# Kernel tuning notes

Measured on AMD Instinct MI355X. Metric: run time of the kernel, lower is better.

## Reference

```python
import jax, jax.numpy as jnp
import numpy as np

N, E, R = 50000, 320000, 3
IN, HID, OUT = 768, 256, 64
NEG_SLOPE = 0.2


def _rgat_conv(x, src, dst, edge_type, W, q, k, bias):
    # x: [N, HID]; W: [R, HID, HID]; q,k: [HID, 1]; bias: [HID]
    n = x.shape[0]
    xw = jnp.einsum('nc,rco->rno', x, W)          # [R, N, HID] per-relation transform
    out_i = xw[edge_type, dst]                      # [E, HID] transformed target feats
    out_j = xw[edge_type, src]                      # [E, HID] transformed source feats
    alpha = jax.nn.leaky_relu(out_i @ q + out_j @ k, NEG_SLOPE)  # [E, 1]
    # across-relation segment softmax over destination nodes (PyG softmax semantics)
    m = jax.ops.segment_max(alpha, dst, num_segments=n)          # [N, 1]
    ea = jnp.exp(alpha - m[dst])
    denom = jax.ops.segment_sum(ea, dst, num_segments=n)         # [N, 1]
    a = ea / (denom[dst] + 1e-16)                                # [E, 1]
    out = jax.ops.segment_sum(a * out_j, dst, num_segments=n)    # [N, HID]
    return out + bias


def setup_inputs() -> dict:
    key = jax.random.key(0)
    ks = jax.random.split(key, 16)
    g = lambda k, shape, fan: (jax.random.normal(k, shape, jnp.float32) / np.float32(np.sqrt(fan)))
    return {
        'x': jax.random.normal(ks[0], (N, IN), jnp.float32),
        'edge_index': jax.random.randint(ks[1], (2, E), 0, N),
        'edge_type': jax.random.randint(ks[2], (E,), 0, R),
        'w_in': g(ks[3], (IN, HID), IN), 'b_in': jnp.zeros((HID,), jnp.float32),
        'conv1_w': g(ks[4], (R, HID, HID), HID),
        'conv1_q': g(ks[5], (HID, 1), HID),
        'conv1_k': g(ks[6], (HID, 1), HID),
        'conv1_b': jnp.zeros((HID,), jnp.float32),
        'conv2_w': g(ks[7], (R, HID, HID), HID),
        'conv2_q': g(ks[8], (HID, 1), HID),
        'conv2_k': g(ks[9], (HID, 1), HID),
        'conv2_b': jnp.zeros((HID,), jnp.float32),
        'w_out': g(ks[10], (HID, OUT), HID), 'b_out': jnp.zeros((OUT,), jnp.float32),
        'w_cls': g(ks[11], (OUT, 2), OUT), 'b_cls': jnp.zeros((2,), jnp.float32),
    }


def reference(x, edge_index, edge_type, w_in, b_in,
              conv1_w, conv1_q, conv1_k, conv1_b,
              conv2_w, conv2_q, conv2_k, conv2_b,
              w_out, b_out, w_cls, b_cls):
    src, dst = edge_index[0], edge_index[1]
    h = jax.nn.relu(x @ w_in + b_in)                                  # [N, HID]
    h = _rgat_conv(h, src, dst, edge_type, conv1_w, conv1_q, conv1_k, conv1_b)
    h = _rgat_conv(h, src, dst, edge_type, conv2_w, conv2_q, conv2_k, conv2_b)
    h = jax.nn.relu(h @ w_out + b_out)                                # [N, OUT]
    return h @ w_cls + b_cls                                          # [N, 2]
```

## Files before the change

### kernel.cpp

```cpp
#include <hip/hip_runtime.h>
#include <hip/hip_bf16.h>

#define RG86_NN 50000
#define RG86_NE 320000
#define RG86_NR 3
#define RG86_DIN 768
#define RG86_HID 256
#define RG86_OUT 64

typedef __bf16 rg_bv8 __attribute__((ext_vector_type(8)));
typedef short rg_sv8 __attribute__((ext_vector_type(8)));
typedef float rg_fv4 __attribute__((ext_vector_type(4)));
typedef unsigned int rg_u32;

static __device__ float rg_b2f(unsigned short u) {
  return __uint_as_float(((unsigned int)u) << 16);
}
static __device__ unsigned short rg_f2b(float f) {
  unsigned int u = __float_as_uint(f);
  u += 0x7FFFu + ((u >> 16) & 1u);
  return (unsigned short)(u >> 16);
}

static __device__ __forceinline__ void rg_gl16(const void* g, void* lds_wave_base) {
  __builtin_amdgcn_global_load_lds(
      (const __attribute__((address_space(1))) rg_u32*)(unsigned long long)(uintptr_t)g,
      (__attribute__((address_space(3))) rg_u32*)(unsigned int)(uintptr_t)lds_wave_base,
      16, 0, 0);
}

__global__ void RGATModel_86371792322702_kernel() {}

__global__ void rg_castT(const float* in, unsigned short* out, int rows, int cols) {
  int i = blockIdx.x * 256 + threadIdx.x;
  if (i < rows * cols) {
    int r = i / cols, c = i % cols;
    out[(size_t)c * rows + r] = rg_f2b(in[i]);
  }
}

__global__ void rg_castT3(const float* in, unsigned short* out) {
  int i = blockIdx.x * 256 + threadIdx.x;
  if (i < RG86_NR * RG86_HID * RG86_HID) {
    int r = i >> 16, j = i & 65535;
    int row = j >> 8, col = j & 255;
    out[(r << 16) + (col << 8) + row] = rg_f2b(in[i]);
  }
}

__global__ void rg_wqk(const float* W, const float* q, const float* k,
                       float* wq, float* wk) {
  int lane = threadIdx.x & 63;
  int p = blockIdx.x * 4 + (threadIdx.x >> 6);
  if (p >= RG86_NR * RG86_HID) return;
  const float* wr = W + (size_t)p * RG86_HID;
  float qv = 0.f, kv = 0.f;
  for (int j = lane; j < RG86_HID; j += 64) {
    float w = wr[j];
    qv += w * q[j];
    kv += w * k[j];
  }
  for (int o = 32; o >= 1; o >>= 1) { qv += __shfl_xor(qv, o); kv += __shfl_xor(kv, o); }
  if (lane == 0) { wq[p] = qv; wk[p] = kv; }
}

__global__ void rg_qk2(const unsigned short* h, const float* wq, const float* wk,
                       float* qd, float* kd) {
  int lane = threadIdx.x & 63;
  int n = blockIdx.x * 4 + (threadIdx.x >> 6);
  if (n >= RG86_NN) return;
  ushort4 hv = *(const ushort4*)(h + (size_t)n * RG86_HID + lane * 4);
  float h0 = rg_b2f(hv.x), h1 = rg_b2f(hv.y), h2 = rg_b2f(hv.z), h3 = rg_b2f(hv.w);
  float acc[6];
#pragma unroll
  for (int r = 0; r < RG86_NR; r++) {
    const float* wqr = wq + r * RG86_HID + lane * 4;
    const float* wkr = wk + r * RG86_HID + lane * 4;
    acc[r] = h0 * wqr[0] + h1 * wqr[1] + h2 * wqr[2] + h3 * wqr[3];
    acc[3 + r] = h0 * wkr[0] + h1 * wkr[1] + h2 * wkr[2] + h3 * wkr[3];
  }
#pragma unroll
  for (int j = 0; j < 6; j++)
    for (int o = 32; o >= 1; o >>= 1) acc[j] += __shfl_xor(acc[j], o);
  if (lane == 0) {
#pragma unroll
    for (int r = 0; r < RG86_NR; r++) {
      qd[r * RG86_NN + n] = acc[r];
      kd[r * RG86_NN + n] = acc[3 + r];
    }
  }
}

__global__ __launch_bounds__(256) void rg_gemm2(
    const unsigned short* A, const unsigned short* Bt, const float* bias,
    unsigned short* C, int M, int N, int K, int relu, int split) {
  __shared__ unsigned short sA[128 * 64];
  __shared__ unsigned short sB[64 * 64];
  int tid = threadIdx.x;
  int wv = tid >> 6, lane = tid & 63;
  int nwg = gridDim.x;
  int q = nwg >> 3, rres = nwg & 7;
  int xcd = blockIdx.x & 7, jj = blockIdx.x >> 3;
  int wg = (xcd < rres ? xcd * (q + 1) : rres * (q + 1) + (xcd - rres) * q) + jj;
  int ntiles = N >> 6;
  int mt = wg / ntiles, nt = wg - mt * ntiles;
  int m0 = mt * 128, n0 = nt * 64;
  int frow = lane & 15, fhi = lane >> 4;
  rg_fv4 acc[2][4] = {};
  for (int k0 = 0; k0 < K; k0 += 64) {
#pragma unroll
    for (int i = 0; i < 4; i++) {
      int idx = i * 256 + tid;
      int r = idx >> 3, s = idx & 7;
      int gr = m0 + r;
      if (gr >= M) gr = M - 1;
      const unsigned short* gp = A + (size_t)gr * K + k0 + ((s ^ (r & 7)) << 3);
      rg_gl16(gp, (char*)sA + (size_t)(i * 256 + wv * 64) * 16);
    }
#pragma unroll
    for (int i = 0; i < 2; i++) {
      int idx = i * 256 + tid;
      int r = idx >> 3, s = idx & 7;
      const unsigned short* gp = Bt + (size_t)(n0 + r) * K + k0 + ((s ^ (r & 7)) << 3);
      rg_gl16(gp, (char*)sB + (size_t)(i * 256 + wv * 64) * 16);
    }
    __syncthreads();
#pragma unroll
    for (int ks = 0; ks < 2; ks++) {
      rg_bv8 af[2], bf[4];
#pragma unroll
      for (int mf = 0; mf < 2; mf++) {
        int r = wv * 32 + mf * 16 + frow;
        int slot = (ks * 4 + fhi) ^ (r & 7);
        af[mf] = *(const rg_bv8*)((const char*)sA + r * 128 + slot * 16);
      }
#pragma unroll
      for (int nf = 0; nf < 4; nf++) {
        int r = nf * 16 + frow;
        int slot = (ks * 4 + fhi) ^ (r & 7);
        bf[nf] = *(const rg_bv8*)((const char*)sB + r * 128 + slot * 16);
      }
#pragma unroll
      for (int mf = 0; mf < 2; mf++)
#pragma unroll
        for (int nf = 0; nf < 4; nf++)
          acc[mf][nf] = __builtin_amdgcn_mfma_f32_16x16x32_bf16(af[mf], bf[nf],
                                                                acc[mf][nf], 0, 0, 0);
    }
    __syncthreads();
  }
#pragma unroll
  for (int mf = 0; mf < 2; mf++) {
#pragma unroll
    for (int nf = 0; nf < 4; nf++) {
      int col = n0 + nf * 16 + frow;
      float bv = bias ? bias[col] : 0.f;
#pragma unroll
      for (int r = 0; r < 4; r++) {
        int row = m0 + wv * 32 + mf * 16 + fhi * 4 + r;
        if (row < M) {
          float v = acc[mf][nf][r] + bv;
          if (relu && v < 0.f) v = 0.f;
          if (split)
            C[((size_t)(col >> 8) * RG86_NN + row) * 256 + (col & 255)] = rg_f2b(v);
          else
            C[(size_t)row * N + col] = rg_f2b(v);
        }
      }
    }
  }
}

__global__ __launch_bounds__(256) void rg_gemm2w(
    const unsigned short* A, const unsigned short* Bt,
    unsigned short* C, int M, int N, int K) {
  __shared__ unsigned short sA[128 * 64];
  __shared__ unsigned short sB[128 * 64];
  int tid = threadIdx.x;
  int wv = tid >> 6, lane = tid & 63;
  int nwg = gridDim.x;
  int q = nwg >> 3, rres = nwg & 7;
  int xcd = blockIdx.x & 7, jj = blockIdx.x >> 3;
  int wg = (xcd < rres ? xcd * (q + 1) : rres * (q + 1) + (xcd - rres) * q) + jj;
  int ntiles = N >> 7;
  int mt = wg / ntiles, nt = wg - mt * ntiles;
  int m0 = mt * 128, n0 = nt * 128;
  int frow = lane & 15, fhi = lane >> 4;
  rg_fv4 acc[2][8] = {};
  for (int k0 = 0; k0 < K; k0 += 64) {
#pragma unroll
    for (int i = 0; i < 4; i++) {
      int idx = i * 256 + tid;
      int r = idx >> 3, s = idx & 7;
      int gr = m0 + r;
      if (gr >= M) gr = M - 1;
      const unsigned short* gp = A + (size_t)gr * K + k0 + ((s ^ (r & 7)) << 3);
      rg_gl16(gp, (char*)sA + (size_t)(i * 256 + wv * 64) * 16);
    }
#pragma unroll
    for (int i = 0; i < 4; i++) {
      int idx = i * 256 + tid;
      int r = idx >> 3, s = idx & 7;
      const unsigned short* gp = Bt + (size_t)(n0 + r) * K + k0 + ((s ^ (r & 7)) << 3);
      rg_gl16(gp, (char*)sB + (size_t)(i * 256 + wv * 64) * 16);
    }
    __syncthreads();
#pragma unroll
    for (int ks = 0; ks < 2; ks++) {
      rg_bv8 af[2], bf[8];
#pragma unroll
      for (int mf = 0; mf < 2; mf++) {
        int r = wv * 32 + mf * 16 + frow;
        int slot = (ks * 4 + fhi) ^ (r & 7);
        af[mf] = *(const rg_bv8*)((const char*)sA + r * 128 + slot * 16);
      }
#pragma unroll
      for (int nf = 0; nf < 8; nf++) {
        int r = nf * 16 + frow;
        int slot = (ks * 4 + fhi) ^ (r & 7);
        bf[nf] = *(const rg_bv8*)((const char*)sB + r * 128 + slot * 16);
      }
#pragma unroll
      for (int mf = 0; mf < 2; mf++)
#pragma unroll
        for (int nf = 0; nf < 8; nf++)
          acc[mf][nf] = __builtin_amdgcn_mfma_f32_16x16x32_bf16(af[mf], bf[nf],
                                                                acc[mf][nf], 0, 0, 0);
    }
    __syncthreads();
  }
#pragma unroll
  for (int mf = 0; mf < 2; mf++) {
#pragma unroll
    for (int nf = 0; nf < 8; nf++) {
      int col = n0 + nf * 16 + frow;
#pragma unroll
      for (int r = 0; r < 4; r++) {
        int row = m0 + wv * 32 + mf * 16 + fhi * 4 + r;
        if (row < M)
          C[((size_t)(col >> 8) * RG86_NN + row) * 256 + (col & 255)] =
              rg_f2b(acc[mf][nf][r]);
      }
    }
  }
}

__global__ __launch_bounds__(256) void rg_gemm2f(
    const float* A, const unsigned short* Bt, const float* bias,
    unsigned short* C, int M, int N, int K, int relu) {
  __shared__ float sA[128 * 64];
  __shared__ unsigned short sB[64 * 64];
  int tid = threadIdx.x;
  int wv = tid >> 6, lane = tid & 63;
  int nwg = gridDim.x;
  int q = nwg >> 3, rres = nwg & 7;
  int xcd = blockIdx.x & 7, jj = blockIdx.x >> 3;
  int wg = (xcd < rres ? xcd * (q + 1) : rres * (q + 1) + (xcd - rres) * q) + jj;
  int ntiles = N >> 6;
  int mt = wg / ntiles, nt = wg - mt * ntiles;
  int m0 = mt * 128, n0 = nt * 64;
  int frow = lane & 15, fhi = lane >> 4;
  rg_fv4 acc[2][4] = {};
  for (int k0 = 0; k0 < K; k0 += 64) {
#pragma unroll
    for (int i = 0; i < 2; i++) {
      int idx = i * 256 + tid;
      int r = idx >> 3, s = idx & 7;
      const unsigned short* gp = Bt + (size_t)(n0 + r) * K + k0 + ((s ^ (r & 7)) << 3);
      rg_gl16(gp, (char*)sB + (size_t)(i * 256 + wv * 64) * 16);
    }
#pragma unroll
    for (int i = 0; i < 8; i++) {
      int idx = i * 256 + tid;
      int r = idx >> 4, hs = idx & 15;
      int gr = m0 + r;
      if (gr >= M) gr = M - 1;
      const float* gp = A + (size_t)gr * K + k0 +
                        ((((hs >> 1) ^ (r & 7)) << 3) + ((hs & 1) << 2));
      rg_gl16(gp, (char*)sA + (size_t)(i * 256 + wv * 64) * 16);
    }
    __syncthreads();
#pragma unroll
    for (int ks = 0; ks < 2; ks++) {
      rg_bv8 af[2], bf[4];
#pragma unroll
      for (int mf = 0; mf < 2; mf++) {
        int r = wv * 32 + mf * 16 + frow;
        int sp = (ks * 4 + fhi) ^ (r & 7);
        const float* ap = sA + r * 64 + sp * 8;
        float4 f0 = *(const float4*)ap;
        float4 f1 = *(const float4*)(ap + 4);
        rg_sv8 av;
        av[0] = (short)rg_f2b(f0.x); av[1] = (short)rg_f2b(f0.y);
        av[2] = (short)rg_f2b(f0.z); av[3] = (short)rg_f2b(f0.w);
        av[4] = (short)rg_f2b(f1.x); av[5] = (short)rg_f2b(f1.y);
        av[6] = (short)rg_f2b(f1.z); av[7] = (short)rg_f2b(f1.w);
        af[mf] = *(rg_bv8*)&av;
      }
#pragma unroll
      for (int nf = 0; nf < 4; nf++) {
        int r = nf * 16 + frow;
        int slot = (ks * 4 + fhi) ^ (r & 7);
        bf[nf] = *(const rg_bv8*)((const char*)sB + r * 128 + slot * 16);
      }
#pragma unroll
      for (int mf = 0; mf < 2; mf++)
#pragma unroll
        for (int nf = 0; nf < 4; nf++)
          acc[mf][nf] = __builtin_amdgcn_mfma_f32_16x16x32_bf16(af[mf], bf[nf],
                                                                acc[mf][nf], 0, 0, 0);
    }
    __syncthreads();
  }
#pragma unroll
  for (int mf = 0; mf < 2; mf++) {
#pragma unroll
    for (int nf = 0; nf < 4; nf++) {
      int col = n0 + nf * 16 + frow;
      float bv = bias ? bias[col] : 0.f;
#pragma unroll
      for (int r = 0; r < 4; r++) {
        int row = m0 + wv * 32 + mf * 16 + fhi * 4 + r;
        if (row < M) {
          float v = acc[mf][nf][r] + bv;
          if (relu && v < 0.f) v = 0.f;
          C[(size_t)row * N + col] = rg_f2b(v);
        }
      }
    }
  }
}

__global__ void rg_hist(const int* d, int* counts) {
  int e = blockIdx.x * 256 + threadIdx.x;
  if (e < RG86_NE) atomicAdd(&counts[d[e]], 1);
}

__global__ void rg_scan1(const int* counts, int* tmp, int* bsum, int n) {
  int b = blockIdx.x, t = threadIdx.x;
  int base = b * 1024 + t * 4;
  int v0 = 0, v1 = 0, v2 = 0, v3 = 0;
  if (base + 3 < n) {
    int4 v = *(const int4*)(counts + base);
    v0 = v.x; v1 = v.y; v2 = v.z; v3 = v.w;
  } else {
    if (base + 0 < n) v0 = counts[base + 0];
    if (base + 1 < n) v1 = counts[base + 1];
    if (base + 2 < n) v2 = counts[base + 2];
    if (base + 3 < n) v3 = counts[base + 3];
  }
  int tsum = v0 + v1 + v2 + v3;
  int lane = t & 63, wave = t >> 6;
  int s = tsum;
  for (int off = 1; off < 64; off <<= 1) {
    int u = __shfl_up(s, off);
    if (lane >= off) s += u;
  }
  __shared__ int wsum[4];
  if (lane == 63) wsum[wave] = s;
  __syncthreads();
  int woff = 0;
  for (int w = 0; w < wave; w++) woff += wsum[w];
  int excl = woff + s - tsum;
  int e0 = excl, e1 = e0 + v0, e2 = e1 + v1, e3 = e2 + v2;
  if (base + 3 < n) {
    *(int4*)(tmp + base) = make_int4(e0, e1, e2, e3);
  } else {
    if (base + 0 < n) tmp[base + 0] = e0;
    if (base + 1 < n) tmp[base + 1] = e1;
    if (base + 2 < n) tmp[base + 2] = e2;
    if (base + 3 < n) tmp[base + 3] = e3;
  }
  if (t == 255) bsum[b] = woff + s;
}

__global__ void rg_scan2(int* bsum, int* rowptr, int nb, int n) {
  int lane = threadIdx.x;
  int v = (lane < nb) ? bsum[lane] : 0;
  int s = v;
  for (int off = 1; off < 64; off <<= 1) {
    int u = __shfl_up(s, off);
    if (lane >= off) s += u;
  }
  if (lane < nb) bsum[lane] = s - v;
  if (lane == 63) rowptr[n] = s;
}

__global__ void rg_scan3(const int* bsum, int* rowptr, int* cursor, int n) {
  int b = blockIdx.x, t = threadIdx.x;
  int base = b * 1024 + t * 4;
  int off = bsum[b];
  if (base + 3 < n) {
    int4 v = *(const int4*)(cursor + base);
    int4 o = make_int4(v.x + off, v.y + off, v.z + off, v.w + off);
    *(int4*)(rowptr + base) = o;
    *(int4*)(cursor + base) = o;
  } else {
    for (int j = 0; j < 4; j++)
      if (base + j < n) {
        int o = cursor[base + j] + off;
        rowptr[base + j] = o;
        cursor[base + j] = o;
      }
  }
}

__global__ void rg_scatter(const int* d, int* cursor, int* perm) {
  int e = blockIdx.x * 256 + threadIdx.x;
  if (e < RG86_NE) perm[atomicAdd(&cursor[d[e]], 1)] = e;
}

__global__ void rg_edge(const int* perm, const int* src, const int* dst,
                        const int* et, const float* qd, const float* kd,
                        float* alphap, int* srcrel) {
  int i = blockIdx.x * 256 + threadIdx.x;
  if (i >= RG86_NE) return;
  int e = perm[i];
  int t = et[e], sv = src[e], dv = dst[e];
  float al = qd[t * RG86_NN + dv] + kd[t * RG86_NN + sv];
  al = al > 0.f ? al : 0.2f * al;
  alphap[i] = al;
  srcrel[i] = t * RG86_NN + sv;
}

__global__ void rg_agg(const int* rowptr, const float* alphap, const int* srcrel,
                       const unsigned short* xw, const float* bias,
                       unsigned short* out) {
  __shared__ float sw[4][64];
  __shared__ int ssrc[4][64];
  int lane = threadIdx.x & 63;
  int wv = threadIdx.x >> 6;
  int node = blockIdx.x * 4 + wv;
  if (node >= RG86_NN) return;
  int s0 = rowptr[node], s1 = rowptr[node + 1];
  int c0 = lane * 4;
  float a0 = 0.f, a1 = 0.f, a2 = 0.f, a3 = 0.f;
  if (s1 > s0) {
    float m = -1e30f;
    for (int bs = s0; bs < s1; bs += 64) {
      int i = bs + lane;
      float al = (i < s1) ? alphap[i] : -1e30f;
      m = fmaxf(m, al);
    }
    for (int o = 32; o >= 1; o >>= 1) m = fmaxf(m, __shfl_xor(m, o));
    float den = 0.f;
    for (int bs = s0; bs < s1; bs += 64) {
      int i = bs + lane;
      if (i < s1) den += __expf(alphap[i] - m);
    }
    for (int o = 32; o >= 1; o >>= 1) den += __shfl_xor(den, o);
    float inv = 1.f / (den + 1e-16f);
    for (int bs = s0; bs < s1; bs += 64) {
      int i = bs + lane;
      int nch = s1 - bs; if (nch > 64) nch = 64;
      float w = 0.f; int sr = 0;
      if (i < s1) { w = __expf(alphap[i] - m) * inv; sr = srcrel[i]; }
      sw[wv][lane] = w;
      ssrc[wv][lane] = sr;
#pragma unroll 4
      for (int j = 0; j < nch; j++) {
        float wj = sw[wv][j];
        ushort4 v = *(const ushort4*)(xw + (size_t)ssrc[wv][j] * RG86_HID + c0);
        a0 += wj * rg_b2f(v.x);
        a1 += wj * rg_b2f(v.y);
        a2 += wj * rg_b2f(v.z);
        a3 += wj * rg_b2f(v.w);
      }
    }
  }
  unsigned short* op = out + (size_t)node * RG86_HID + c0;
  op[0] = rg_f2b(a0 + bias[c0 + 0]);
  op[1] = rg_f2b(a1 + bias[c0 + 1]);
  op[2] = rg_f2b(a2 + bias[c0 + 2]);
  op[3] = rg_f2b(a3 + bias[c0 + 3]);
}

__global__ void rg_cls(const unsigned short* h4, const float* wc, const float* bc,
                       float* out) {
  int n = blockIdx.x * 256 + threadIdx.x;
  if (n >= RG86_NN) return;
  float a0 = bc[0], a1 = bc[1];
  const unsigned short* hr = h4 + (size_t)n * RG86_OUT;
  for (int j = 0; j < RG86_OUT; j++) {
    float h = rg_b2f(hr[j]);
    a0 += h * wc[j * 2 + 0];
    a1 += h * wc[j * 2 + 1];
  }
  out[n * 2 + 0] = a0;
  out[n * 2 + 1] = a1;
}

extern "C" void kernel_launch(void* const* d_in, const int* in_sizes, int n_in,
                              void* d_out, int out_size, void* d_ws, size_t ws_size,
                              hipStream_t stream) {
  (void)in_sizes; (void)n_in; (void)out_size;
  const float* x = (const float*)d_in[0];
  const int* ei = (const int*)d_in[1];
  const int* etp = (const int*)d_in[2];
  const float* w_in = (const float*)d_in[3];
  const float* b_in = (const float*)d_in[4];
  const float* c1w = (const float*)d_in[5];
  const float* c1q = (const float*)d_in[6];
  const float* c1k = (const float*)d_in[7];
  const float* c1b = (const float*)d_in[8];
  const float* c2w = (const float*)d_in[9];
  const float* c2q = (const float*)d_in[10];
  const float* c2k = (const float*)d_in[11];
  const float* c2b = (const float*)d_in[12];
  const float* w_out = (const float*)d_in[13];
  const float* b_out = (const float*)d_in[14];
  const float* w_cls = (const float*)d_in[15];
  const float* b_cls = (const float*)d_in[16];
  const int* esrc = ei;
  const int* edst = ei + RG86_NE;

  char* base = (char*)d_ws;
  size_t off = 0;
  unsigned short* xw = (unsigned short*)(base + off);
  off += (size_t)RG86_NR * RG86_NN * RG86_HID * 2;
  unsigned short* h1b = (unsigned short*)(base + off); off += (size_t)RG86_NN * RG86_HID * 2;
  unsigned short* h2b = (unsigned short*)(base + off); off += (size_t)RG86_NN * RG86_HID * 2;
  unsigned short* h4b = (unsigned short*)(base + off); off += (size_t)RG86_NN * RG86_OUT * 2;
  unsigned short* w_inT = (unsigned short*)(base + off); off += (size_t)RG86_DIN * RG86_HID * 2;
  unsigned short* c1wT = (unsigned short*)(base + off); off += (size_t)RG86_NR * RG86_HID * RG86_HID * 2;
  unsigned short* c2wT = (unsigned short*)(base + off); off += (size_t)RG86_NR * RG86_HID * RG86_HID * 2;
  unsigned short* w_outT = (unsigned short*)(base + off); off += (size_t)RG86_HID * RG86_OUT * 2;
  float* qd = (float*)(base + off); off += (size_t)RG86_NR * RG86_NN * 4;
  float* kd = (float*)(base + off); off += (size_t)RG86_NR * RG86_NN * 4;
  float* wq1 = (float*)(base + off); off += (size_t)RG86_NR * RG86_HID * 4;
  float* wk1 = (float*)(base + off); off += (size_t)RG86_NR * RG86_HID * 4;
  float* wq2 = (float*)(base + off); off += (size_t)RG86_NR * RG86_HID * 4;
  float* wk2 = (float*)(base + off); off += (size_t)RG86_NR * RG86_HID * 4;
  int* counts = (int*)(base + off); off += (size_t)RG86_NN * 4;
  int* rowptr = (int*)(base + off); off += (size_t)(RG86_NN + 4) * 4;
  int* cursor = (int*)(base + off); off += (size_t)RG86_NN * 4;
  int* perm = (int*)(base + off); off += (size_t)RG86_NE * 4;
  int* bsum = (int*)(base + off); off += (size_t)64 * 4;
  float* alphap = (float*)(base + off); off += (size_t)RG86_NE * 4;
  int* srcrel = (int*)(base + off); off += (size_t)RG86_NE * 4;
  if (off > ws_size) return;

  int mt128 = (RG86_NN + 127) / 128;
  int nsb = (RG86_NN + 1023) / 1024;

  rg_castT<<<(RG86_DIN * RG86_HID + 255) / 256, 256, 0, stream>>>(
      w_in, w_inT, RG86_DIN, RG86_HID);
  rg_castT3<<<(RG86_NR * RG86_HID * RG86_HID + 255) / 256, 256, 0, stream>>>(c1w, c1wT);
  rg_castT3<<<(RG86_NR * RG86_HID * RG86_HID + 255) / 256, 256, 0, stream>>>(c2w, c2wT);
  rg_castT<<<(RG86_HID * RG86_OUT + 255) / 256, 256, 0, stream>>>(
      w_out, w_outT, RG86_HID, RG86_OUT);
  rg_wqk<<<(RG86_NR * RG86_HID + 3) / 4, 256, 0, stream>>>(c1w, c1q, c1k, wq1, wk1);
  rg_wqk<<<(RG86_NR * RG86_HID + 3) / 4, 256, 0, stream>>>(c2w, c2q, c2k, wq2, wk2);

  rg_gemm2f<<<mt128 * 4, 256, 0, stream>>>(x, w_inT, b_in, h1b,
                                           RG86_NN, RG86_HID, RG86_DIN, 1);

  hipMemsetAsync(counts, 0, (size_t)RG86_NN * 4, stream);
  rg_hist<<<(RG86_NE + 255) / 256, 256, 0, stream>>>(edst, counts);
  rg_scan1<<<nsb, 256, 0, stream>>>(counts, cursor, bsum, RG86_NN);
  rg_scan2<<<1, 64, 0, stream>>>(bsum, rowptr, nsb, RG86_NN);
  rg_scan3<<<nsb, 256, 0, stream>>>(bsum, rowptr, cursor, RG86_NN);
  rg_scatter<<<(RG86_NE + 255) / 256, 256, 0, stream>>>(edst, cursor, perm);

  rg_gemm2w<<<mt128 * 6, 256, 0, stream>>>(h1b, c1wT, xw,
                                           RG86_NN, RG86_NR * RG86_HID, RG86_HID);
  rg_qk2<<<(RG86_NN + 3) / 4, 256, 0, stream>>>(h1b, wq1, wk1, qd, kd);
  rg_edge<<<(RG86_NE + 255) / 256, 256, 0, stream>>>(perm, esrc, edst, etp, qd, kd,
                                                     alphap, srcrel);
  rg_agg<<<(RG86_NN + 3) / 4, 256, 0, stream>>>(rowptr, alphap, srcrel,
                                                xw, c1b, h2b);

  rg_gemm2w<<<mt128 * 6, 256, 0, stream>>>(h2b, c2wT, xw,
                                           RG86_NN, RG86_NR * RG86_HID, RG86_HID);
  rg_qk2<<<(RG86_NN + 3) / 4, 256, 0, stream>>>(h2b, wq2, wk2, qd, kd);
  rg_edge<<<(RG86_NE + 255) / 256, 256, 0, stream>>>(perm, esrc, edst, etp, qd, kd,
                                                     alphap, srcrel);
  rg_agg<<<(RG86_NN + 3) / 4, 256, 0, stream>>>(rowptr, alphap, srcrel,
                                                xw, c2b, h1b);

  rg_gemm2<<<mt128, 256, 0, stream>>>(h1b, w_outT, b_out, h4b,
                                      RG86_NN, RG86_OUT, RG86_HID, 1, 0);

  rg_cls<<<(RG86_NN + 255) / 256, 256, 0, stream>>>(h4b, w_cls, b_cls, (float*)d_out);
}
```

Baseline: 571.3 us.

## Fuse output GEMM with classifier and widen input GEMM N-tile to 128

The final 256->64 GEMM now applies bias and ReLU in registers, multiplies by the 64x2 classifier weights, and reduces across lanes to write the [N,2] output directly. This removes the intermediate h4 buffer round trip and the separate classifier kernel. Separately, the fp32-input first GEMM tile grows from 128x64 to 128x128, so the fp32 A tile is loaded and converted once per two N-tiles instead of four. The wider tile costs more registers and LDS per block and halves the block count.

```diff
diff --git a/kernel.cpp b/kernel.cpp
--- a/kernel.cpp
+++ b/kernel.cpp
@@ -87,86 +87,6 @@
     for (int r = 0; r < RG86_NR; r++) {
       qd[r * RG86_NN + n] = acc[r];
       kd[r * RG86_NN + n] = acc[3 + r];
-    }
-  }
-}
-
-__global__ __launch_bounds__(256) void rg_gemm2(
-    const unsigned short* A, const unsigned short* Bt, const float* bias,
-    unsigned short* C, int M, int N, int K, int relu, int split) {
-  __shared__ unsigned short sA[128 * 64];
-  __shared__ unsigned short sB[64 * 64];
-  int tid = threadIdx.x;
-  int wv = tid >> 6, lane = tid & 63;
-  int nwg = gridDim.x;
-  int q = nwg >> 3, rres = nwg & 7;
-  int xcd = blockIdx.x & 7, jj = blockIdx.x >> 3;
-  int wg = (xcd < rres ? xcd * (q + 1) : rres * (q + 1) + (xcd - rres) * q) + jj;
-  int ntiles = N >> 6;
-  int mt = wg / ntiles, nt = wg - mt * ntiles;
-  int m0 = mt * 128, n0 = nt * 64;
-  int frow = lane & 15, fhi = lane >> 4;
-  rg_fv4 acc[2][4] = {};
-  for (int k0 = 0; k0 < K; k0 += 64) {
-#pragma unroll
-    for (int i = 0; i < 4; i++) {
-      int idx = i * 256 + tid;
-      int r = idx >> 3, s = idx & 7;
-      int gr = m0 + r;
-      if (gr >= M) gr = M - 1;
-      const unsigned short* gp = A + (size_t)gr * K + k0 + ((s ^ (r & 7)) << 3);
-      rg_gl16(gp, (char*)sA + (size_t)(i * 256 + wv * 64) * 16);
-    }
-#pragma unroll
-    for (int i = 0; i < 2; i++) {
-      int idx = i * 256 + tid;
-      int r = idx >> 3, s = idx & 7;
-      const unsigned short* gp = Bt + (size_t)(n0 + r) * K + k0 + ((s ^ (r & 7)) << 3);
-      rg_gl16(gp, (char*)sB + (size_t)(i * 256 + wv * 64) * 16);
-    }
-    __syncthreads();
-#pragma unroll
-    for (int ks = 0; ks < 2; ks++) {
-      rg_bv8 af[2], bf[4];
-#pragma unroll
-      for (int mf = 0; mf < 2; mf++) {
-        int r = wv * 32 + mf * 16 + frow;
-        int slot = (ks * 4 + fhi) ^ (r & 7);
-        af[mf] = *(const rg_bv8*)((const char*)sA + r * 128 + slot * 16);
-      }
-#pragma unroll
-      for (int nf = 0; nf < 4; nf++) {
-        int r = nf * 16 + frow;
-        int slot = (ks * 4 + fhi) ^ (r & 7);
-        bf[nf] = *(const rg_bv8*)((const char*)sB + r * 128 + slot * 16);
-      }
-#pragma unroll
-      for (int mf = 0; mf < 2; mf++)
-#pragma unroll
-        for (int nf = 0; nf < 4; nf++)
-          acc[mf][nf] = __builtin_amdgcn_mfma_f32_16x16x32_bf16(af[mf], bf[nf],
-                                                                acc[mf][nf], 0, 0, 0);
-    }
-    __syncthreads();
-  }
-#pragma unroll
-  for (int mf = 0; mf < 2; mf++) {
-#pragma unroll
-    for (int nf = 0; nf < 4; nf++) {
-      int col = n0 + nf * 16 + frow;
-      float bv = bias ? bias[col] : 0.f;
-#pragma unroll
-      for (int r = 0; r < 4; r++) {
-        int row = m0 + wv * 32 + mf * 16 + fhi * 4 + r;
-        if (row < M) {
-          float v = acc[mf][nf][r] + bv;
-          if (relu && v < 0.f) v = 0.f;
-          if (split)
-            C[((size_t)(col >> 8) * RG86_NN + row) * 256 + (col & 255)] = rg_f2b(v);
-          else
-            C[(size_t)row * N + col] = rg_f2b(v);
-        }
-      }
     }
   }
 }
@@ -249,21 +169,21 @@
     const float* A, const unsigned short* Bt, const float* bias,
     unsigned short* C, int M, int N, int K, int relu) {
   __shared__ float sA[128 * 64];
-  __shared__ unsigned short sB[64 * 64];
+  __shared__ unsigned short sB[128 * 64];
   int tid = threadIdx.x;
   int wv = tid >> 6, lane = tid & 63;
   int nwg = gridDim.x;
   int q = nwg >> 3, rres = nwg & 7;
   int xcd = blockIdx.x & 7, jj = blockIdx.x >> 3;
   int wg = (xcd < rres ? xcd * (q + 1) : rres * (q + 1) + (xcd - rres) * q) + jj;
-  int ntiles = N >> 6;
+  int ntiles = N >> 7;
   int mt = wg / ntiles, nt = wg - mt * ntiles;
-  int m0 = mt * 128, n0 = nt * 64;
+  int m0 = mt * 128, n0 = nt * 128;
   int frow = lane & 15, fhi = lane >> 4;
-  rg_fv4 acc[2][4] = {};
+  rg_fv4 acc[2][8] = {};
   for (int k0 = 0; k0 < K; k0 += 64) {
 #pragma unroll
-    for (int i = 0; i < 2; i++) {
+    for (int i = 0; i < 4; i++) {
       int idx = i * 256 + tid;
       int r = idx >> 3, s = idx & 7;
       const unsigned short* gp = Bt + (size_t)(n0 + r) * K + k0 + ((s ^ (r & 7)) << 3);
@@ -282,7 +202,7 @@
     __syncthreads();
 #pragma unroll
     for (int ks = 0; ks < 2; ks++) {
-      rg_bv8 af[2], bf[4];
+      rg_bv8 af[2], bf[8];
 #pragma unroll
       for (int mf = 0; mf < 2; mf++) {
         int r = wv * 32 + mf * 16 + frow;
@@ -298,7 +218,7 @@
         af[mf] = *(rg_bv8*)&av;
       }
 #pragma unroll
-      for (int nf = 0; nf < 4; nf++) {
+      for (int nf = 0; nf < 8; nf++) {
         int r = nf * 16 + frow;
         int slot = (ks * 4 + fhi) ^ (r & 7);
         bf[nf] = *(const rg_bv8*)((const char*)sB + r * 128 + slot * 16);
@@ -306,7 +226,7 @@
 #pragma unroll
       for (int mf = 0; mf < 2; mf++)
 #pragma unroll
-        for (int nf = 0; nf < 4; nf++)
+        for (int nf = 0; nf < 8; nf++)
           acc[mf][nf] = __builtin_amdgcn_mfma_f32_16x16x32_bf16(af[mf], bf[nf],
                                                                 acc[mf][nf], 0, 0, 0);
     }
@@ -315,7 +235,7 @@
 #pragma unroll
   for (int mf = 0; mf < 2; mf++) {
 #pragma unroll
-    for (int nf = 0; nf < 4; nf++) {
+    for (int nf = 0; nf < 8; nf++) {
       int col = n0 + nf * 16 + frow;
       float bv = bias ? bias[col] : 0.f;
 #pragma unroll
@@ -326,6 +246,87 @@
           if (relu && v < 0.f) v = 0.f;
           C[(size_t)row * N + col] = rg_f2b(v);
         }
+      }
+    }
+  }
+}
+
+__global__ __launch_bounds__(256) void rg_gemm2c(
+    const unsigned short* A, const unsigned short* Bt, const float* bias,
+    const float* wc, const float* bc, float* out, int M, int K) {
+  __shared__ unsigned short sA[128 * 64];
+  __shared__ unsigned short sB[64 * 64];
+  int tid = threadIdx.x;
+  int wv = tid >> 6, lane = tid & 63;
+  int mt = blockIdx.x;
+  int m0 = mt * 128;
+  int frow = lane & 15, fhi = lane >> 4;
+  rg_fv4 acc[2][4] = {};
+  for (int k0 = 0; k0 < K; k0 += 64) {
+#pragma unroll
+    for (int i = 0; i < 4; i++) {
+      int idx = i * 256 + tid;
+      int r = idx >> 3, s = idx & 7;
+      int gr = m0 + r;
+      if (gr >= M) gr = M - 1;
+      const unsigned short* gp = A + (size_t)gr * K + k0 + ((s ^ (r & 7)) << 3);
+      rg_gl16(gp, (char*)sA + (size_t)(i * 256 + wv * 64) * 16);
+    }
+#pragma unroll
+    for (int i = 0; i < 2; i++) {
+      int idx = i * 256 + tid;
+      int r = idx >> 3, s = idx & 7;
+      const unsigned short* gp = Bt + (size_t)r * K + k0 + ((s ^ (r & 7)) << 3);
+      rg_gl16(gp, (char*)sB + (size_t)(i * 256 + wv * 64) * 16);
+    }
+    __syncthreads();
+#pragma unroll
+    for (int ks = 0; ks < 2; ks++) {
+      rg_bv8 af[2], bf[4];
+#pragma unroll
+      for (int mf = 0; mf < 2; mf++) {
+        int r = wv * 32 + mf * 16 + frow;
+        int slot = (ks * 4 + fhi) ^ (r & 7);
+        af[mf] = *(const rg_bv8*)((const char*)sA + r * 128 + slot * 16);
+      }
+#pragma unroll
+      for (int nf = 0; nf < 4; nf++) {
+        int r = nf * 16 + frow;
+        int slot = (ks * 4 + fhi) ^ (r & 7);
+        bf[nf] = *(const rg_bv8*)((const char*)sB + r * 128 + slot * 16);
+      }
+#pragma unroll
+      for (int mf = 0; mf < 2; mf++)
+#pragma unroll
+        for (int nf = 0; nf < 4; nf++)
+          acc[mf][nf] = __builtin_amdgcn_mfma_f32_16x16x32_bf16(af[mf], bf[nf],
+                                                                acc[mf][nf], 0, 0, 0);
+    }
+    __syncthreads();
+  }
+  float bc0 = bc[0], bc1 = bc[1];
+#pragma unroll
+  for (int mf = 0; mf < 2; mf++) {
+#pragma unroll
+    for (int r = 0; r < 4; r++) {
+      float p0 = 0.f, p1 = 0.f;
+#pragma unroll
+      for (int nf = 0; nf < 4; nf++) {
+        int col = nf * 16 + frow;
+        float v = acc[mf][nf][r] + bias[col];
+        if (v < 0.f) v = 0.f;
+        p0 += v * wc[col * 2 + 0];
+        p1 += v * wc[col * 2 + 1];
+      }
+#pragma unroll
+      for (int o = 1; o < 16; o <<= 1) {
+        p0 += __shfl_xor(p0, o);
+        p1 += __shfl_xor(p1, o);
+      }
+      int row = m0 + wv * 32 + mf * 16 + fhi * 4 + r;
+      if (frow == 0 && row < M) {
+        out[row * 2 + 0] = p0 + bc0;
+        out[row * 2 + 1] = p1 + bc1;
       }
     }
   }
@@ -473,21 +474,6 @@
   op[1] = rg_f2b(a1 + bias[c0 + 1]);
   op[2] = rg_f2b(a2 + bias[c0 + 2]);
   op[3] = rg_f2b(a3 + bias[c0 + 3]);
-}
-
-__global__ void rg_cls(const unsigned short* h4, const float* wc, const float* bc,
-                       float* out) {
-  int n = blockIdx.x * 256 + threadIdx.x;
-  if (n >= RG86_NN) return;
-  float a0 = bc[0], a1 = bc[1];
-  const unsigned short* hr = h4 + (size_t)n * RG86_OUT;
-  for (int j = 0; j < RG86_OUT; j++) {
-    float h = rg_b2f(hr[j]);
-    a0 += h * wc[j * 2 + 0];
-    a1 += h * wc[j * 2 + 1];
-  }
-  out[n * 2 + 0] = a0;
-  out[n * 2 + 1] = a1;
 }
 
 extern "C" void kernel_launch(void* const* d_in, const int* in_sizes, int n_in,
@@ -520,7 +506,6 @@
   off += (size_t)RG86_NR * RG86_NN * RG86_HID * 2;
   unsigned short* h1b = (unsigned short*)(base + off); off += (size_t)RG86_NN * RG86_HID * 2;
   unsigned short* h2b = (unsigned short*)(base + off); off += (size_t)RG86_NN * RG86_HID * 2;
-  unsigned short* h4b = (unsigned short*)(base + off); off += (size_t)RG86_NN * RG86_OUT * 2;
   unsigned short* w_inT = (unsigned short*)(base + off); off += (size_t)RG86_DIN * RG86_HID * 2;
   unsigned short* c1wT = (unsigned short*)(base + off); off += (size_t)RG86_NR * RG86_HID * RG86_HID * 2;
   unsigned short* c2wT = (unsigned short*)(base + off); off += (size_t)RG86_NR * RG86_HID * RG86_HID * 2;
@@ -552,7 +537,7 @@
   rg_wqk<<<(RG86_NR * RG86_HID + 3) / 4, 256, 0, stream>>>(c1w, c1q, c1k, wq1, wk1);
   rg_wqk<<<(RG86_NR * RG86_HID + 3) / 4, 256, 0, stream>>>(c2w, c2q, c2k, wq2, wk2);
 
-  rg_gemm2f<<<mt128 * 4, 256, 0, stream>>>(x, w_inT, b_in, h1b,
+  rg_gemm2f<<<mt128 * 2, 256, 0, stream>>>(x, w_inT, b_in, h1b,
                                            RG86_NN, RG86_HID, RG86_DIN, 1);
 
   hipMemsetAsync(counts, 0, (size_t)RG86_NN * 4, stream);
@@ -578,8 +563,6 @@
   rg_agg<<<(RG86_NN + 3) / 4, 256, 0, stream>>>(rowptr, alphap, srcrel,
                                                 xw, c2b, h1b);
 
-  rg_gemm2<<<mt128, 256, 0, stream>>>(h1b, w_outT, b_out, h4b,
-                                      RG86_NN, RG86_OUT, RG86_HID, 1, 0);
-
-  rg_cls<<<(RG86_NN + 255) / 256, 256, 0, stream>>>(h4b, w_cls, b_cls, (float*)d_out);
-}
+  rg_gemm2c<<<mt128, 256, 0, stream>>>(h1b, w_outT, b_out, w_cls, b_cls,
+                                       (float*)d_out, RG86_NN, RG86_HID);
+}
```

Measured after the change: 569.8 us. About the same (-0.3%).
